# Optimization experiments

Hardware: AMD Instinct MI355X
Metric: run time of the kernel (lower is better)

Reference implementation:

```python
import jax, jax.numpy as jnp
import numpy as np

N = 50000
E = 800000
IN_FEATS = 256
NUM_HEADS = 4
OUT_FEATS = 64
NUM_ETYPES = 8
ALPHA = 100.0
NEG_SLOPE_ATTN = 0.2   # self.leaky_relu
NEG_SLOPE_EW = 0.01    # nn.LeakyReLU() default, applied to edge weights


def leaky_relu(x, slope):
    return jnp.where(x >= 0, x, slope * x)


def setup_inputs() -> dict:
    key = jax.random.key(0)
    ks = jax.random.split(key, 8)
    feat = jax.random.normal(ks[0], (N, IN_FEATS), dtype=jnp.float32)
    src = jax.random.randint(ks[1], (E,), 0, N, dtype=jnp.int32)
    dst = jax.random.randint(ks[2], (E,), 0, N, dtype=jnp.int32)
    # etypes are 1-indexed in the original code (edge_weight[edge_feats - 1])
    edge_feats = jax.random.randint(ks[3], (E,), 1, NUM_ETYPES + 1, dtype=jnp.int32)
    # parameters (xavier-normal-ish init for weights; edge_weight = 1/alpha)
    fc_w = jax.random.normal(ks[4], (NUM_HEADS * OUT_FEATS, IN_FEATS), dtype=jnp.float32) * 0.05
    attn_l = jax.random.normal(ks[5], (1, NUM_HEADS, OUT_FEATS), dtype=jnp.float32) * 0.1
    attn_r = jax.random.normal(ks[6], (1, NUM_HEADS, OUT_FEATS), dtype=jnp.float32) * 0.1
    edge_weight = jnp.full((NUM_ETYPES, NUM_HEADS), 1.0 / ALPHA, dtype=jnp.float32)
    return {"feat": feat, "src": src, "dst": dst, "edge_feats": edge_feats,
            "fc_w": fc_w, "attn_l": attn_l, "attn_r": attn_r, "edge_weight": edge_weight}


def reference(feat, src, dst, edge_feats, fc_w, attn_l, attn_r, edge_weight):
    # feat: [N, F_in] -> ft: [N, H, D]
    ft = (feat @ fc_w.T).reshape(-1, NUM_HEADS, OUT_FEATS)
    el = jnp.einsum('nhd,ohd->nh', ft, attn_l)  # [N, H]
    er = jnp.einsum('nhd,ohd->nh', ft, attn_r)  # [N, H]
    # edge-type weights (1-indexed), scaled & leaky-relu'd
    ew = leaky_relu(edge_weight * ALPHA, NEG_SLOPE_EW)  # [T, H]
    ee = ew[edge_feats - 1]                              # [E, H]
    # per-edge logits: u_add_v, times edge weight, leaky relu
    e = leaky_relu((el[src] + er[dst]) * ee, NEG_SLOPE_ATTN)  # [E, H]
    # edge softmax grouped by destination node
    emax = jax.ops.segment_max(e, dst, num_segments=N)        # [N, H]
    ex = jnp.exp(e - emax[dst])
    denom = jax.ops.segment_sum(ex, dst, num_segments=N)      # [N, H]
    a = ex / denom[dst]                                        # [E, H]
    # weighted scatter-sum: sum over edges of a * ft[src]
    msg = ft[src] * a[:, :, None]                              # [E, H, D]
    rst = jax.ops.segment_sum(msg, dst, num_segments=N)       # [N, H, D]
    return rst
```

## Files before the change

### kernel.cpp

```cpp
#include <hip/hip_runtime.h>
#include <hip/hip_bf16.h>


#define NF 256
#define HD 256
#define NH 4

typedef __attribute__((ext_vector_type(8))) short short8;
typedef __attribute__((ext_vector_type(4))) float f32x4;

static __device__ __forceinline__ unsigned short f2bf(float f) {
  unsigned int u = __float_as_uint(f);
  u += 0x7FFFu + ((u >> 16) & 1u);
  return (unsigned short)(u >> 16);
}
static __device__ __forceinline__ float bf2f(unsigned short s) {
  return __uint_as_float(((unsigned int)s) << 16);
}
static __device__ __forceinline__ unsigned pkbf(float a, float b) {
  __hip_bfloat162 h = __float22bfloat162_rn(make_float2(a, b));
  return *(unsigned*)&h;
}

__global__ __launch_bounds__(256) void hist_cvt_rank_k(
    const int* __restrict__ dst, int* __restrict__ cursor,
    int* __restrict__ rank, const float* __restrict__ w,
    unsigned short* __restrict__ o, int e) {
  int i = blockIdx.x * 256 + threadIdx.x;
  if (i < 16384) {
    float4 v = ((const float4*)w)[i];
    ((uint2*)o)[i] = make_uint2(pkbf(v.x, v.y), pkbf(v.z, v.w));
  }
  if (i < e) rank[i] = atomicAdd(&cursor[dst[i]], 1);
}

__global__ __launch_bounds__(1024) void scan_k(const int* __restrict__ cursor,
                                               int* __restrict__ offs, int n) {
  __shared__ int wtot[16];
  __shared__ int wexcl[16];
  __shared__ int ctot;
  int tid = threadIdx.x, lane = tid & 63, wid = tid >> 6;
  int carry = 0;
  int nchunk = (n + 8191) >> 13;
  for (int c = 0; c < nchunk; ++c) {
    int base = (c << 13) + tid * 8;
    int v[8];
    if (base + 8 <= n) {
      int4 a = *(const int4*)(cursor + base);
      int4 b = *(const int4*)(cursor + base + 4);
      v[0] = a.x; v[1] = a.y; v[2] = a.z; v[3] = a.w;
      v[4] = b.x; v[5] = b.y; v[6] = b.z; v[7] = b.w;
    } else {
#pragma unroll
      for (int j = 0; j < 8; ++j) v[j] = (base + j < n) ? cursor[base + j] : 0;
    }
    int p[8]; int run = 0;
#pragma unroll
    for (int j = 0; j < 8; ++j) { run += v[j]; p[j] = run; }
    int incl = run;
#pragma unroll
    for (int off = 1; off < 64; off <<= 1) {
      int t = __shfl_up(incl, off);
      if (lane >= off) incl += t;
    }
    if (lane == 63) wtot[wid] = incl;
    __syncthreads();
    if (wid == 0 && lane < 16) {
      int wv = wtot[lane]; int wi = wv;
#pragma unroll
      for (int off = 1; off < 16; off <<= 1) {
        int t = __shfl_up(wi, off);
        if (lane >= off) wi += t;
      }
      wexcl[lane] = wi - wv;
      if (lane == 15) ctot = wi;
    }
    __syncthreads();
    int ebase = carry + wexcl[wid] + (incl - run);
#pragma unroll
    for (int j = 0; j < 8; ++j) {
      int i = base + j;
      if (i < n) offs[i] = ebase + p[j] - v[j];
    }
    carry += ctot;
    __syncthreads();
  }
  if (tid == 0) offs[n] = carry;
}

__global__ __launch_bounds__(256) void gemm_k(
    const float* __restrict__ feat, const unsigned short* __restrict__ fcb,
    const float* __restrict__ attn_l, const float* __restrict__ attn_r,
    unsigned short* __restrict__ ftb, float* __restrict__ el,
    float* __restrict__ er, int n) {
  __shared__ short aF[4 * 2 * 64 * 8];
  __shared__ short bF[16 * 2 * 64 * 8];
  int tid = threadIdx.x;
  int lane = tid & 63, w = tid >> 6;
  int row0 = blockIdx.x * 64;

  f32x4 acc[4][4];
#pragma unroll
  for (int i = 0; i < 4; ++i)
#pragma unroll
    for (int j = 0; j < 4; ++j) acc[i][j] = (f32x4){0.f, 0.f, 0.f, 0.f};

  int ar = tid >> 2, ak = (tid & 3) << 4;
  int arow = row0 + ar; if (arow >= n) arow = n - 1;
  const float* ap = feat + (size_t)arow * NF + ak;
  int am = ar & 15, art = ar >> 4;
  int s0 = ak >> 5, q0 = (ak >> 3) & 3;
  int s1 = (ak + 8) >> 5, q1 = ((ak + 8) >> 3) & 3;
  short* aw0 = &aF[(((art * 2 + s0) * 64) + q0 * 16 + am) * 8];
  short* aw1 = &aF[(((art * 2 + s1) * 64) + q1 * 16 + am) * 8];

  const unsigned short* bp = fcb + (size_t)tid * NF;
  int bn = tid & 15, bcg = tid >> 4;

  for (int k0 = 0; k0 < NF; k0 += 64) {
    float4 f0 = *(const float4*)(ap + k0);
    float4 f1 = *(const float4*)(ap + k0 + 4);
    float4 f2 = *(const float4*)(ap + k0 + 8);
    float4 f3 = *(const float4*)(ap + k0 + 12);
    uint4 oa = make_uint4(pkbf(f0.x, f0.y), pkbf(f0.z, f0.w),
                          pkbf(f1.x, f1.y), pkbf(f1.z, f1.w));
    uint4 ob = make_uint4(pkbf(f2.x, f2.y), pkbf(f2.z, f2.w),
                          pkbf(f3.x, f3.y), pkbf(f3.z, f3.w));
    *(uint4*)aw0 = oa;
    *(uint4*)aw1 = ob;
#pragma unroll
    for (int o8 = 0; o8 < 8; ++o8) {
      short8 bv = *(const short8*)(bp + k0 + o8 * 8);
      int bs = o8 >> 2, bq = o8 & 3;
      *(short8*)&bF[(((bcg * 2 + bs) * 64) + bq * 16 + bn) * 8] = bv;
    }
    __syncthreads();
#pragma unroll
    for (int s = 0; s < 2; ++s) {
      short8 af[4], bfr[4];
#pragma unroll
      for (int rt = 0; rt < 4; ++rt)
        af[rt] = *(const short8*)&aF[(((rt * 2 + s) * 64) + lane) * 8];
#pragma unroll
      for (int ct = 0; ct < 4; ++ct)
        bfr[ct] = *(const short8*)&bF[((((w * 4 + ct) * 2 + s) * 64) + lane) * 8];
#pragma unroll
      for (int rt = 0; rt < 4; ++rt)
#pragma unroll
        for (int ct = 0; ct < 4; ++ct)
          acc[rt][ct] = __builtin_amdgcn_mfma_f32_16x16x32_bf16(
              af[rt], bfr[ct], acc[rt][ct], 0, 0, 0);
    }
    __syncthreads();
  }

  int ln = lane & 15, lq = lane >> 4;
  float al4[4], ar4[4];
#pragma unroll
  for (int ct = 0; ct < 4; ++ct) {
    al4[ct] = attn_l[w * 64 + ct * 16 + ln];
    ar4[ct] = attn_r[w * 64 + ct * 16 + ln];
  }
#pragma unroll
  for (int rt = 0; rt < 4; ++rt) {
#pragma unroll
    for (int r = 0; r < 4; ++r) {
      float pl = 0.f, pr = 0.f;
#pragma unroll
      for (int ct = 0; ct < 4; ++ct) {
        float v = acc[rt][ct][r];
        pl += v * al4[ct]; pr += v * ar4[ct];
      }
#pragma unroll
      for (int off = 1; off <= 8; off <<= 1) {
        pl += __shfl_xor(pl, off);
        pr += __shfl_xor(pr, off);
      }
      int row = row0 + rt * 16 + lq * 4 + r;
      if (row < n) {
        if (ln == 0) { el[row * NH + w] = pl; er[row * NH + w] = pr; }
        unsigned short* fr = ftb + (size_t)row * HD + w * 64 + ln;
#pragma unroll
        for (int ct = 0; ct < 4; ++ct) fr[ct * 16] = f2bf(acc[rt][ct][r]);
      }
    }
  }
}

__global__ __launch_bounds__(256) void scatter4_k(
    const int* __restrict__ src, const int* __restrict__ dst,
    const int* __restrict__ efeats, const int* __restrict__ rank,
    const int* __restrict__ offs, const float* __restrict__ el,
    const float* __restrict__ er, const float* __restrict__ ewt,
    int* __restrict__ srcs_g, float4* __restrict__ exq, int e) {
  __shared__ float ew_s[32];
  if (threadIdx.x < 32) {
    float v = ewt[threadIdx.x] * 100.0f;
    ew_s[threadIdx.x] = (v >= 0.f) ? v : 0.01f * v;
  }
  __syncthreads();
  int i = blockIdx.x * 256 + threadIdx.x;
  if (i >= e) return;
  int d = dst[i], s = src[i], t = efeats[i] - 1;
  int p = offs[d] + rank[i];
  float4 elv = *(const float4*)(el + (size_t)s * 4);
  float4 erv = *(const float4*)(er + (size_t)d * 4);
  const float* ew = &ew_s[t * 4];
  float x0 = (elv.x + erv.x) * ew[0]; x0 = (x0 >= 0.f) ? x0 : 0.2f * x0;
  float x1 = (elv.y + erv.y) * ew[1]; x1 = (x1 >= 0.f) ? x1 : 0.2f * x1;
  float x2 = (elv.z + erv.z) * ew[2]; x2 = (x2 >= 0.f) ? x2 : 0.2f * x2;
  float x3 = (elv.w + erv.w) * ew[3]; x3 = (x3 >= 0.f) ? x3 : 0.2f * x3;
  exq[p] = make_float4(__expf(x0), __expf(x1), __expf(x2), __expf(x3));
  srcs_g[p] = s;
}

__global__ __launch_bounds__(256) void agg2_k(
    const unsigned short* __restrict__ ftb, const int* __restrict__ srcs_g,
    const float4* __restrict__ exq, const int* __restrict__ offs,
    float* __restrict__ out, int n) {
  int node = blockIdx.x * 4 + (threadIdx.x >> 6);
  int lane = threadIdx.x & 63;
  if (node >= n) return;
  int start = offs[node];
  int deg = offs[node + 1] - start;
  float o0 = 0.f, o1 = 0.f, o2 = 0.f, o3 = 0.f;
  if (deg > 0) {
    float s0 = 0.f, s1 = 0.f, s2 = 0.f, s3 = 0.f;
    for (int i = lane; i < deg; i += 64) {
      float4 q = exq[(size_t)start + i];
      s0 += q.x; s1 += q.y; s2 += q.z; s3 += q.w;
    }
#pragma unroll
    for (int off = 1; off < 64; off <<= 1) {
      s0 += __shfl_xor(s0, off);
      s1 += __shfl_xor(s1, off);
      s2 += __shfl_xor(s2, off);
      s3 += __shfl_xor(s3, off);
    }
    int hl = lane >> 4;
    float sh = (hl == 0) ? s0 : (hl == 1) ? s1 : (hl == 2) ? s2 : s3;
    float rs = 1.0f / sh;
    const float* exs = (const float*)exq;
    const unsigned short* fb = ftb + (size_t)lane * 4;
    const int* sg = srcs_g + start;
    long b4 = (long)start * 4 + hl;
    int i = 0;
    for (; i + 8 <= deg; i += 8) {
      int sA = sg[i],     sB = sg[i + 1], sC = sg[i + 2], sD = sg[i + 3];
      int sE = sg[i + 4], sF = sg[i + 5], sG = sg[i + 6], sH = sg[i + 7];
      ushort4 fA = *(const ushort4*)(fb + (size_t)sA * HD);
      ushort4 fB = *(const ushort4*)(fb + (size_t)sB * HD);
      ushort4 fC = *(const ushort4*)(fb + (size_t)sC * HD);
      ushort4 fD = *(const ushort4*)(fb + (size_t)sD * HD);
      ushort4 fE = *(const ushort4*)(fb + (size_t)sE * HD);
      ushort4 fF = *(const ushort4*)(fb + (size_t)sF * HD);
      ushort4 fG = *(const ushort4*)(fb + (size_t)sG * HD);
      ushort4 fH = *(const ushort4*)(fb + (size_t)sH * HD);
      float wA = exs[b4 + (long)i * 4]       * rs;
      float wB = exs[b4 + (long)(i + 1) * 4] * rs;
      float wC = exs[b4 + (long)(i + 2) * 4] * rs;
      float wD = exs[b4 + (long)(i + 3) * 4] * rs;
      float wE = exs[b4 + (long)(i + 4) * 4] * rs;
      float wF = exs[b4 + (long)(i + 5) * 4] * rs;
      float wG = exs[b4 + (long)(i + 6) * 4] * rs;
      float wH = exs[b4 + (long)(i + 7) * 4] * rs;
      o0 = fmaf(wA, bf2f(fA.x), o0); o1 = fmaf(wA, bf2f(fA.y), o1);
      o2 = fmaf(wA, bf2f(fA.z), o2); o3 = fmaf(wA, bf2f(fA.w), o3);
      o0 = fmaf(wB, bf2f(fB.x), o0); o1 = fmaf(wB, bf2f(fB.y), o1);
      o2 = fmaf(wB, bf2f(fB.z), o2); o3 = fmaf(wB, bf2f(fB.w), o3);
      o0 = fmaf(wC, bf2f(fC.x), o0); o1 = fmaf(wC, bf2f(fC.y), o1);
      o2 = fmaf(wC, bf2f(fC.z), o2); o3 = fmaf(wC, bf2f(fC.w), o3);
      o0 = fmaf(wD, bf2f(fD.x), o0); o1 = fmaf(wD, bf2f(fD.y), o1);
      o2 = fmaf(wD, bf2f(fD.z), o2); o3 = fmaf(wD, bf2f(fD.w), o3);
      o0 = fmaf(wE, bf2f(fE.x), o0); o1 = fmaf(wE, bf2f(fE.y), o1);
      o2 = fmaf(wE, bf2f(fE.z), o2); o3 = fmaf(wE, bf2f(fE.w), o3);
      o0 = fmaf(wF, bf2f(fF.x), o0); o1 = fmaf(wF, bf2f(fF.y), o1);
      o2 = fmaf(wF, bf2f(fF.z), o2); o3 = fmaf(wF, bf2f(fF.w), o3);
      o0 = fmaf(wG, bf2f(fG.x), o0); o1 = fmaf(wG, bf2f(fG.y), o1);
      o2 = fmaf(wG, bf2f(fG.z), o2); o3 = fmaf(wG, bf2f(fG.w), o3);
      o0 = fmaf(wH, bf2f(fH.x), o0); o1 = fmaf(wH, bf2f(fH.y), o1);
      o2 = fmaf(wH, bf2f(fH.z), o2); o3 = fmaf(wH, bf2f(fH.w), o3);
    }
    for (; i < deg; ++i) {
      int sA = sg[i];
      float wA = exs[b4 + (long)i * 4] * rs;
      ushort4 fA = *(const ushort4*)(fb + (size_t)sA * HD);
      o0 = fmaf(wA, bf2f(fA.x), o0); o1 = fmaf(wA, bf2f(fA.y), o1);
      o2 = fmaf(wA, bf2f(fA.z), o2); o3 = fmaf(wA, bf2f(fA.w), o3);
    }
  }
  *(float4*)(out + (size_t)node * HD + lane * 4) = make_float4(o0, o1, o2, o3);
}

extern "C" void kernel_launch(void* const* d_in, const int* in_sizes, int n_in,
                              void* d_out, int out_size, void* d_ws, size_t ws_size,
                              hipStream_t stream) {
  const float* feat   = (const float*)d_in[0];
  const int*   src    = (const int*)d_in[1];
  const int*   dst    = (const int*)d_in[2];
  const int*   efeats = (const int*)d_in[3];
  const float* fc_w   = (const float*)d_in[4];
  const float* attn_l = (const float*)d_in[5];
  const float* attn_r = (const float*)d_in[6];
  const float* ewt    = (const float*)d_in[7];
  float* out = (float*)d_out;

  int N = in_sizes[0] / NF;
  int E = in_sizes[1];

  char* ws = (char*)d_ws;
  size_t off = 0;
  unsigned short* fcb = (unsigned short*)(ws + off); off += (size_t)NF * HD * 2;
  unsigned short* ftb = (unsigned short*)(ws + off); off += (size_t)N * HD * 2;
  float* el  = (float*)(ws + off);  off += (size_t)N * NH * 4;
  float* er  = (float*)(ws + off);  off += (size_t)N * NH * 4;
  int* offs  = (int*)(ws + off);    off += ((size_t)N + 16) * 4;
  int* cursor = (int*)(ws + off);   off += (size_t)N * 4;
  int* rank  = (int*)(ws + off);    off += (size_t)E * 4;
  int* srcs_g = (int*)(ws + off);   off += (size_t)E * 4;
  float4* exq = (float4*)(ws + off); off += (size_t)E * 16;

  hipMemsetAsync(cursor, 0, (size_t)N * 4, stream);
  hist_cvt_rank_k<<<(E + 255) / 256, 256, 0, stream>>>(dst, cursor, rank, fc_w, fcb, E);
  scan_k<<<1, 1024, 0, stream>>>(cursor, offs, N);
  gemm_k<<<(N + 63) / 64, 256, 0, stream>>>(feat, fcb, attn_l, attn_r, ftb, el, er, N);
  scatter4_k<<<(E + 255) / 256, 256, 0, stream>>>(src, dst, efeats, rank, offs,
                                                  el, er, ewt, srcs_g, exq, E);
  agg2_k<<<(N + 3) / 4, 256, 0, stream>>>(ftb, srcs_g, exq, offs, out, N);
}
```

Measured before the change: 304.0 us.

## Store edge exp weights in fp16, halve GEMM row tile, shorten aggregation unroll

Edge softmax numerators are now stored as packed fp16 (8 bytes per edge instead of 16), which halves the write traffic in the scatter pass and the read traffic in aggregation. The GEMM row tile drops from 64 to 32 rows per block, giving twice as many blocks with fewer accumulators each. The aggregation gather loop unroll goes from 8 to 4. fp16 exp values risk overflow or precision loss when logits are large, and the smaller GEMM tile re-reads the weight matrix into shared memory more often.

After: 306.9 us. Within noise of the previous version (+0.9%).

```diff
diff --git a/kernel.cpp b/kernel.cpp
--- a/kernel.cpp
+++ b/kernel.cpp
@@ -1,5 +1,6 @@
 #include <hip/hip_runtime.h>
 #include <hip/hip_bf16.h>
+#include <hip/hip_fp16.h>
 
 
 #define NF 256
@@ -19,6 +20,10 @@
 }
 static __device__ __forceinline__ unsigned pkbf(float a, float b) {
   __hip_bfloat162 h = __float22bfloat162_rn(make_float2(a, b));
+  return *(unsigned*)&h;
+}
+static __device__ __forceinline__ unsigned pk2h(float a, float b) {
+  __half2 h = __floats2half2_rn(a, b);
   return *(unsigned*)&h;
 }
 
@@ -93,26 +98,24 @@
     const float* __restrict__ attn_l, const float* __restrict__ attn_r,
     unsigned short* __restrict__ ftb, float* __restrict__ el,
     float* __restrict__ er, int n) {
-  __shared__ short aF[4 * 2 * 64 * 8];
+  __shared__ short aF[2 * 2 * 64 * 8];
   __shared__ short bF[16 * 2 * 64 * 8];
   int tid = threadIdx.x;
   int lane = tid & 63, w = tid >> 6;
-  int row0 = blockIdx.x * 64;
-
-  f32x4 acc[4][4];
-#pragma unroll
-  for (int i = 0; i < 4; ++i)
+  int row0 = blockIdx.x * 32;
+
+  f32x4 acc[2][4];
+#pragma unroll
+  for (int i = 0; i < 2; ++i)
 #pragma unroll
     for (int j = 0; j < 4; ++j) acc[i][j] = (f32x4){0.f, 0.f, 0.f, 0.f};
 
-  int ar = tid >> 2, ak = (tid & 3) << 4;
+  int ar = tid >> 3, ak = (tid & 7) << 3;
   int arow = row0 + ar; if (arow >= n) arow = n - 1;
   const float* ap = feat + (size_t)arow * NF + ak;
   int am = ar & 15, art = ar >> 4;
   int s0 = ak >> 5, q0 = (ak >> 3) & 3;
-  int s1 = (ak + 8) >> 5, q1 = ((ak + 8) >> 3) & 3;
   short* aw0 = &aF[(((art * 2 + s0) * 64) + q0 * 16 + am) * 8];
-  short* aw1 = &aF[(((art * 2 + s1) * 64) + q1 * 16 + am) * 8];
 
   const unsigned short* bp = fcb + (size_t)tid * NF;
   int bn = tid & 15, bcg = tid >> 4;
@@ -120,14 +123,9 @@
   for (int k0 = 0; k0 < NF; k0 += 64) {
     float4 f0 = *(const float4*)(ap + k0);
     float4 f1 = *(const float4*)(ap + k0 + 4);
-    float4 f2 = *(const float4*)(ap + k0 + 8);
-    float4 f3 = *(const float4*)(ap + k0 + 12);
     uint4 oa = make_uint4(pkbf(f0.x, f0.y), pkbf(f0.z, f0.w),
                           pkbf(f1.x, f1.y), pkbf(f1.z, f1.w));
-    uint4 ob = make_uint4(pkbf(f2.x, f2.y), pkbf(f2.z, f2.w),
-                          pkbf(f3.x, f3.y), pkbf(f3.z, f3.w));
     *(uint4*)aw0 = oa;
-    *(uint4*)aw1 = ob;
 #pragma unroll
     for (int o8 = 0; o8 < 8; ++o8) {
       short8 bv = *(const short8*)(bp + k0 + o8 * 8);
@@ -137,15 +135,15 @@
     __syncthreads();
 #pragma unroll
     for (int s = 0; s < 2; ++s) {
-      short8 af[4], bfr[4];
-#pragma unroll
-      for (int rt = 0; rt < 4; ++rt)
+      short8 af[2], bfr[4];
+#pragma unroll
+      for (int rt = 0; rt < 2; ++rt)
         af[rt] = *(const short8*)&aF[(((rt * 2 + s) * 64) + lane) * 8];
 #pragma unroll
       for (int ct = 0; ct < 4; ++ct)
         bfr[ct] = *(const short8*)&bF[((((w * 4 + ct) * 2 + s) * 64) + lane) * 8];
 #pragma unroll
-      for (int rt = 0; rt < 4; ++rt)
+      for (int rt = 0; rt < 2; ++rt)
 #pragma unroll
         for (int ct = 0; ct < 4; ++ct)
           acc[rt][ct] = __builtin_amdgcn_mfma_f32_16x16x32_bf16(
@@ -162,7 +160,7 @@
     ar4[ct] = attn_r[w * 64 + ct * 16 + ln];
   }
 #pragma unroll
-  for (int rt = 0; rt < 4; ++rt) {
+  for (int rt = 0; rt < 2; ++rt) {
 #pragma unroll
     for (int r = 0; r < 4; ++r) {
       float pl = 0.f, pr = 0.f;
@@ -192,7 +190,7 @@
     const int* __restrict__ efeats, const int* __restrict__ rank,
     const int* __restrict__ offs, const float* __restrict__ el,
     const float* __restrict__ er, const float* __restrict__ ewt,
-    int* __restrict__ srcs_g, float4* __restrict__ exq, int e) {
+    int* __restrict__ srcs_g, uint2* __restrict__ exq, int e) {
   __shared__ float ew_s[32];
   if (threadIdx.x < 32) {
     float v = ewt[threadIdx.x] * 100.0f;
@@ -210,13 +208,13 @@
   float x1 = (elv.y + erv.y) * ew[1]; x1 = (x1 >= 0.f) ? x1 : 0.2f * x1;
   float x2 = (elv.z + erv.z) * ew[2]; x2 = (x2 >= 0.f) ? x2 : 0.2f * x2;
   float x3 = (elv.w + erv.w) * ew[3]; x3 = (x3 >= 0.f) ? x3 : 0.2f * x3;
-  exq[p] = make_float4(__expf(x0), __expf(x1), __expf(x2), __expf(x3));
+  exq[p] = make_uint2(pk2h(__expf(x0), __expf(x1)), pk2h(__expf(x2), __expf(x3)));
   srcs_g[p] = s;
 }
 
 __global__ __launch_bounds__(256) void agg2_k(
     const unsigned short* __restrict__ ftb, const int* __restrict__ srcs_g,
-    const float4* __restrict__ exq, const int* __restrict__ offs,
+    const uint2* __restrict__ exq, const int* __restrict__ offs,
     float* __restrict__ out, int n) {
   int node = blockIdx.x * 4 + (threadIdx.x >> 6);
   int lane = threadIdx.x & 63;
@@ -227,8 +225,10 @@
   if (deg > 0) {
     float s0 = 0.f, s1 = 0.f, s2 = 0.f, s3 = 0.f;
     for (int i = lane; i < deg; i += 64) {
-      float4 q = exq[(size_t)start + i];
-      s0 += q.x; s1 += q.y; s2 += q.z; s3 += q.w;
+      uint2 q = exq[(size_t)start + i];
+      float2 f01 = __half22float2(*(__half2*)&q.x);
+      float2 f23 = __half22float2(*(__half2*)&q.y);
+      s0 += f01.x; s1 += f01.y; s2 += f23.x; s3 += f23.y;
     }
 #pragma unroll
     for (int off = 1; off < 64; off <<= 1) {
@@ -240,30 +240,21 @@
     int hl = lane >> 4;
     float sh = (hl == 0) ? s0 : (hl == 1) ? s1 : (hl == 2) ? s2 : s3;
     float rs = 1.0f / sh;
-    const float* exs = (const float*)exq;
+    const __half* exs = (const __half*)exq;
     const unsigned short* fb = ftb + (size_t)lane * 4;
     const int* sg = srcs_g + start;
     long b4 = (long)start * 4 + hl;
     int i = 0;
-    for (; i + 8 <= deg; i += 8) {
-      int sA = sg[i],     sB = sg[i + 1], sC = sg[i + 2], sD = sg[i + 3];
-      int sE = sg[i + 4], sF = sg[i + 5], sG = sg[i + 6], sH = sg[i + 7];
+    for (; i + 4 <= deg; i += 4) {
+      int sA = sg[i], sB = sg[i + 1], sC = sg[i + 2], sD = sg[i + 3];
+      float wA = __half2float(exs[b4 + (long)i * 4])       * rs;
+      float wB = __half2float(exs[b4 + (long)(i + 1) * 4]) * rs;
+      float wC = __half2float(exs[b4 + (long)(i + 2) * 4]) * rs;
+      float wD = __half2float(exs[b4 + (long)(i + 3) * 4]) * rs;
       ushort4 fA = *(const ushort4*)(fb + (size_t)sA * HD);
       ushort4 fB = *(const ushort4*)(fb + (size_t)sB * HD);
       ushort4 fC = *(const ushort4*)(fb + (size_t)sC * HD);
       ushort4 fD = *(const ushort4*)(fb + (size_t)sD * HD);
-      ushort4 fE = *(const ushort4*)(fb + (size_t)sE * HD);
-      ushort4 fF = *(const ushort4*)(fb + (size_t)sF * HD);
-      ushort4 fG = *(const ushort4*)(fb + (size_t)sG * HD);
-      ushort4 fH = *(const ushort4*)(fb + (size_t)sH * HD);
-      float wA = exs[b4 + (long)i * 4]       * rs;
-      float wB = exs[b4 + (long)(i + 1) * 4] * rs;
-      float wC = exs[b4 + (long)(i + 2) * 4] * rs;
-      float wD = exs[b4 + (long)(i + 3) * 4] * rs;
-      float wE = exs[b4 + (long)(i + 4) * 4] * rs;
-      float wF = exs[b4 + (long)(i + 5) * 4] * rs;
-      float wG = exs[b4 + (long)(i + 6) * 4] * rs;
-      float wH = exs[b4 + (long)(i + 7) * 4] * rs;
       o0 = fmaf(wA, bf2f(fA.x), o0); o1 = fmaf(wA, bf2f(fA.y), o1);
       o2 = fmaf(wA, bf2f(fA.z), o2); o3 = fmaf(wA, bf2f(fA.w), o3);
       o0 = fmaf(wB, bf2f(fB.x), o0); o1 = fmaf(wB, bf2f(fB.y), o1);
@@ -272,18 +263,10 @@
       o2 = fmaf(wC, bf2f(fC.z), o2); o3 = fmaf(wC, bf2f(fC.w), o3);
       o0 = fmaf(wD, bf2f(fD.x), o0); o1 = fmaf(wD, bf2f(fD.y), o1);
       o2 = fmaf(wD, bf2f(fD.z), o2); o3 = fmaf(wD, bf2f(fD.w), o3);
-      o0 = fmaf(wE, bf2f(fE.x), o0); o1 = fmaf(wE, bf2f(fE.y), o1);
-      o2 = fmaf(wE, bf2f(fE.z), o2); o3 = fmaf(wE, bf2f(fE.w), o3);
-      o0 = fmaf(wF, bf2f(fF.x), o0); o1 = fmaf(wF, bf2f(fF.y), o1);
-      o2 = fmaf(wF, bf2f(fF.z), o2); o3 = fmaf(wF, bf2f(fF.w), o3);
-      o0 = fmaf(wG, bf2f(fG.x), o0); o1 = fmaf(wG, bf2f(fG.y), o1);
-      o2 = fmaf(wG, bf2f(fG.z), o2); o3 = fmaf(wG, bf2f(fG.w), o3);
-      o0 = fmaf(wH, bf2f(fH.x), o0); o1 = fmaf(wH, bf2f(fH.y), o1);
-      o2 = fmaf(wH, bf2f(fH.z), o2); o3 = fmaf(wH, bf2f(fH.w), o3);
     }
     for (; i < deg; ++i) {
       int sA = sg[i];
-      float wA = exs[b4 + (long)i * 4] * rs;
+      float wA = __half2float(exs[b4 + (long)i * 4]) * rs;
       ushort4 fA = *(const ushort4*)(fb + (size_t)sA * HD);
       o0 = fmaf(wA, bf2f(fA.x), o0); o1 = fmaf(wA, bf2f(fA.y), o1);
       o2 = fmaf(wA, bf2f(fA.z), o2); o3 = fmaf(wA, bf2f(fA.w), o3);
@@ -318,12 +301,12 @@
   int* cursor = (int*)(ws + off);   off += (size_t)N * 4;
   int* rank  = (int*)(ws + off);    off += (size_t)E * 4;
   int* srcs_g = (int*)(ws + off);   off += (size_t)E * 4;
-  float4* exq = (float4*)(ws + off); off += (size_t)E * 16;
+  uint2* exq = (uint2*)(ws + off);  off += (size_t)E * 8;
 
   hipMemsetAsync(cursor, 0, (size_t)N * 4, stream);
   hist_cvt_rank_k<<<(E + 255) / 256, 256, 0, stream>>>(dst, cursor, rank, fc_w, fcb, E);
   scan_k<<<1, 1024, 0, stream>>>(cursor, offs, N);
-  gemm_k<<<(N + 63) / 64, 256, 0, stream>>>(feat, fcb, attn_l, attn_r, ftb, el, er, N);
+  gemm_k<<<(N + 31) / 32, 256, 0, stream>>>(feat, fcb, attn_l, attn_r, ftb, el, er, N);
   scatter4_k<<<(E + 255) / 256, 256, 0, stream>>>(src, dst, efeats, rank, offs,
                                                   el, er, ewt, srcs_g, exq, E);
   agg2_k<<<(N + 3) / 4, 256, 0, stream>>>(ftb, srcs_g, exq, offs, out, N);
```
